# Performance work log

Measured on AMD Instinct MI355X. Metric: run time of the kernel, lower is better.

## Reference

```python
import jax, jax.numpy as jnp
import numpy as np

NEG_BIG = -1e9


def setup_inputs() -> dict:
    key = jax.random.key(0)
    ks = jax.random.split(key, 6)
    B, Tq, Tv, D, A = 4, 256, 1024, 512, 128
    inputs = jax.random.normal(ks[0], (B, Tv, D), dtype=jnp.float32)
    context = jax.random.normal(ks[1], (B, Tq, D), dtype=jnp.float32)
    mask = jnp.ones((B, Tv), dtype=jnp.int32)  # 1 = valid position
    scale = 1.0 / np.sqrt(D)
    Wk = jax.random.normal(ks[2], (D, A), dtype=jnp.float32) * scale
    bk = jnp.zeros((A,), dtype=jnp.float32)
    Wq = jax.random.normal(ks[3], (D, A), dtype=jnp.float32) * scale
    bq = jnp.zeros((A,), dtype=jnp.float32)
    attn_v = jax.random.normal(ks[4], (A,), dtype=jnp.float32) * (1.0 / np.sqrt(A))
    return {"inputs": inputs, "context": context, "mask": mask,
            "Wk": Wk, "bk": bk, "Wq": Wq, "bq": bq, "attn_v": attn_v}


def reference(inputs, context, mask, Wk, bk, Wq, bq, attn_v):
    # inputs: [B,Tv,D] (keys/values), context: [B,Tq,D] (queries)
    k = jnp.einsum('bvd,da->bva', inputs, Wk) + bk        # [B,Tv,A]
    q = jnp.einsum('bqd,da->bqa', context, Wq) + bq       # [B,Tq,A]
    # additive (Bahdanau) score: sum_a v_a * tanh(q + k)
    t = jnp.tanh(q[:, :, None, :] + k[:, None, :, :])     # [B,Tq,Tv,A]
    scores = jnp.einsum('bqva,a->bqv', t, attn_v)         # [B,Tq,Tv]
    neg = (1.0 - mask.astype(jnp.float32))[:, None, :] * NEG_BIG
    scores = scores + neg
    attn = jax.nn.softmax(scores, axis=-1)                # [B,Tq,Tv]
    return jnp.einsum('bqv,bvd->bqd', attn, inputs)       # [B,Tq,D]
```

## Files before the change

### kernel.cpp

```cpp
#include <hip/hip_runtime.h>
#include <math.h>

#define B   4
#define TQ  256
#define TV  1024
#define D   512
#define A   128

#define LOG2E     1.4426950408889634f
#define TWO_LOG2E 2.8853900817779268f
#define NEG_BIG_F (-1e9f)

#define QBLK (B * TQ / 8)
#define KBLK (B * TV / 8)

__global__ __launch_bounds__(256, 4) void proj_exp_kernel(
    const float* __restrict__ ctx, const float* __restrict__ inp,
    const float* __restrict__ Wq, const float* __restrict__ bq,
    const float* __restrict__ Wk, const float* __restrict__ bk,
    float* __restrict__ Eq, float* __restrict__ EkT) {
  __shared__ float ps[8][4][A];
  __shared__ float es[A][9];

  bool isQ = blockIdx.x < QBLK;
  const float* X; const float* W; const float* bias; int r0;
  if (isQ) { X = ctx; W = Wq; bias = bq; r0 = blockIdx.x * 8; }
  else     { X = inp; W = Wk; bias = bk; r0 = (blockIdx.x - QBLK) * 8; }

  int tid = threadIdx.x;
  int ap = (tid & 63) * 2;
  int g  = tid >> 6;

  int dbase = __builtin_amdgcn_readfirstlane(g * 128);
  const float* Xr = X + (size_t)r0 * D + dbase;
  const float* Wd = W + (size_t)dbase * A + ap;

  float2 acc[8];
#pragma unroll
  for (int j = 0; j < 8; ++j) acc[j] = make_float2(0.f, 0.f);

#pragma unroll 2
  for (int dd = 0; dd < 128; dd += 4) {
    float2 w0 = *(const float2*)(Wd + (size_t)(dd + 0) * A);
    float2 w1 = *(const float2*)(Wd + (size_t)(dd + 1) * A);
    float2 w2 = *(const float2*)(Wd + (size_t)(dd + 2) * A);
    float2 w3 = *(const float2*)(Wd + (size_t)(dd + 3) * A);
    float4 x[8];
#pragma unroll
    for (int j = 0; j < 8; ++j)
      x[j] = *(const float4*)(Xr + (size_t)j * D + dd);
#pragma unroll
    for (int j = 0; j < 8; ++j) {
      acc[j].x = fmaf(x[j].x, w0.x, acc[j].x);
      acc[j].y = fmaf(x[j].x, w0.y, acc[j].y);
      acc[j].x = fmaf(x[j].y, w1.x, acc[j].x);
      acc[j].y = fmaf(x[j].y, w1.y, acc[j].y);
      acc[j].x = fmaf(x[j].z, w2.x, acc[j].x);
      acc[j].y = fmaf(x[j].z, w2.y, acc[j].y);
      acc[j].x = fmaf(x[j].w, w3.x, acc[j].x);
      acc[j].y = fmaf(x[j].w, w3.y, acc[j].y);
    }
  }

#pragma unroll
  for (int j = 0; j < 8; ++j)
    *(float2*)&ps[j][g][ap] = acc[j];
  __syncthreads();

  int j  = tid >> 5;
  int a4 = (tid & 31) * 4;
  float4 p0 = *(const float4*)&ps[j][0][a4];
  float4 p1 = *(const float4*)&ps[j][1][a4];
  float4 p2 = *(const float4*)&ps[j][2][a4];
  float4 p3 = *(const float4*)&ps[j][3][a4];
  float4 bz = *(const float4*)(bias + a4);
  float4 ev;
  ev.x = __builtin_amdgcn_exp2f((((p0.x + p1.x) + (p2.x + p3.x)) + bz.x) * TWO_LOG2E);
  ev.y = __builtin_amdgcn_exp2f((((p0.y + p1.y) + (p2.y + p3.y)) + bz.y) * TWO_LOG2E);
  ev.z = __builtin_amdgcn_exp2f((((p0.z + p1.z) + (p2.z + p3.z)) + bz.z) * TWO_LOG2E);
  ev.w = __builtin_amdgcn_exp2f((((p0.w + p1.w) + (p2.w + p3.w)) + bz.w) * TWO_LOG2E);

  if (isQ) {
    *(float4*)(Eq + (size_t)(r0 + j) * A + a4) = ev;
  } else {
    es[a4 + 0][j] = ev.x;
    es[a4 + 1][j] = ev.y;
    es[a4 + 2][j] = ev.z;
    es[a4 + 3][j] = ev.w;
    __syncthreads();
    int b  = r0 >> 10;
    int v0 = r0 & (TV - 1);
    for (int i = tid; i < A * 8; i += 256) {
      int aa = i >> 3, jj = i & 7;
      EkT[((size_t)b * A + aa) * TV + v0 + jj] = es[aa][jj];
    }
  }
}

__global__ __launch_bounds__(512, 4) void score_softmax_kernel(
    const float* __restrict__ Eq, const float* __restrict__ EkT,
    const float* __restrict__ attn_v, const int* __restrict__ mask,
    float* __restrict__ attn) {
  __shared__ float redA[8], redB[8];
  __shared__ float bc[4];

  int tid = threadIdx.x;
  int v0  = (tid & 63) * 2 + (tid >> 6) * 128;
  int r0  = blockIdx.x * 2;
  int b   = r0 >> 8;

  const float* eqA = Eq + (size_t)r0 * A;
  const float* eqB = eqA + A;

  float sumV = 0.f;
#pragma unroll 16
  for (int i = 0; i < A; ++i) sumV += attn_v[i];

  const float* ekb = EkT + (size_t)b * A * TV + v0;
  float2 tA = make_float2(0.f, 0.f);
  float2 tB = make_float2(0.f, 0.f);

  float2 c0 = *(const float2*)(ekb + (size_t)0 * TV);
  float2 c1 = *(const float2*)(ekb + (size_t)1 * TV);
  float2 c2 = *(const float2*)(ekb + (size_t)2 * TV);
  float2 c3 = *(const float2*)(ekb + (size_t)3 * TV);

  for (int i = 0; i < A; i += 4) {
    float2 n0, n1, n2, n3;
    if (i < A - 4) {
      n0 = *(const float2*)(ekb + (size_t)(i + 4) * TV);
      n1 = *(const float2*)(ekb + (size_t)(i + 5) * TV);
      n2 = *(const float2*)(ekb + (size_t)(i + 6) * TV);
      n3 = *(const float2*)(ekb + (size_t)(i + 7) * TV);
    }
    float av0 = attn_v[i + 0], av1 = attn_v[i + 1];
    float av2 = attn_v[i + 2], av3 = attn_v[i + 3];
    float qa0 = eqA[i + 0], qa1 = eqA[i + 1], qa2 = eqA[i + 2], qa3 = eqA[i + 3];
    float qb0 = eqB[i + 0], qb1 = eqB[i + 1], qb2 = eqB[i + 2], qb3 = eqB[i + 3];

    tA.x = fmaf(av0, __builtin_amdgcn_rcpf(fmaf(c0.x, qa0, 1.f)), tA.x);
    tA.y = fmaf(av0, __builtin_amdgcn_rcpf(fmaf(c0.y, qa0, 1.f)), tA.y);
    tB.x = fmaf(av0, __builtin_amdgcn_rcpf(fmaf(c0.x, qb0, 1.f)), tB.x);
    tB.y = fmaf(av0, __builtin_amdgcn_rcpf(fmaf(c0.y, qb0, 1.f)), tB.y);

    tA.x = fmaf(av1, __builtin_amdgcn_rcpf(fmaf(c1.x, qa1, 1.f)), tA.x);
    tA.y = fmaf(av1, __builtin_amdgcn_rcpf(fmaf(c1.y, qa1, 1.f)), tA.y);
    tB.x = fmaf(av1, __builtin_amdgcn_rcpf(fmaf(c1.x, qb1, 1.f)), tB.x);
    tB.y = fmaf(av1, __builtin_amdgcn_rcpf(fmaf(c1.y, qb1, 1.f)), tB.y);

    tA.x = fmaf(av2, __builtin_amdgcn_rcpf(fmaf(c2.x, qa2, 1.f)), tA.x);
    tA.y = fmaf(av2, __builtin_amdgcn_rcpf(fmaf(c2.y, qa2, 1.f)), tA.y);
    tB.x = fmaf(av2, __builtin_amdgcn_rcpf(fmaf(c2.x, qb2, 1.f)), tB.x);
    tB.y = fmaf(av2, __builtin_amdgcn_rcpf(fmaf(c2.y, qb2, 1.f)), tB.y);

    tA.x = fmaf(av3, __builtin_amdgcn_rcpf(fmaf(c3.x, qa3, 1.f)), tA.x);
    tA.y = fmaf(av3, __builtin_amdgcn_rcpf(fmaf(c3.y, qa3, 1.f)), tA.y);
    tB.x = fmaf(av3, __builtin_amdgcn_rcpf(fmaf(c3.x, qb3, 1.f)), tB.x);
    tB.y = fmaf(av3, __builtin_amdgcn_rcpf(fmaf(c3.y, qb3, 1.f)), tB.y);

    c0 = n0; c1 = n1; c2 = n2; c3 = n3;
  }

  int2 mk = *(const int2*)(mask + b * TV + v0);
  float mkx = (1.f - (float)mk.x) * NEG_BIG_F;
  float mky = (1.f - (float)mk.y) * NEG_BIG_F;
  float2 sA, sB;
  sA.x = sumV - 2.f * tA.x + mkx;
  sA.y = sumV - 2.f * tA.y + mky;
  sB.x = sumV - 2.f * tB.x + mkx;
  sB.y = sumV - 2.f * tB.y + mky;

  float mA = fmaxf(sA.x, sA.y);
  float mB = fmaxf(sB.x, sB.y);
  for (int off = 32; off > 0; off >>= 1) {
    mA = fmaxf(mA, __shfl_down(mA, off, 64));
    mB = fmaxf(mB, __shfl_down(mB, off, 64));
  }
  int w = tid >> 6;
  if ((tid & 63) == 0) { redA[w] = mA; redB[w] = mB; }
  __syncthreads();
  if (tid == 0) {
    float a = redA[0], bm = redB[0];
#pragma unroll
    for (int i = 1; i < 8; ++i) { a = fmaxf(a, redA[i]); bm = fmaxf(bm, redB[i]); }
    bc[0] = a; bc[1] = bm;
  }
  __syncthreads();
  float MA = bc[0], MB = bc[1];

  float2 eAv, eBv;
  eAv.x = __builtin_amdgcn_exp2f((sA.x - MA) * LOG2E);
  eAv.y = __builtin_amdgcn_exp2f((sA.y - MA) * LOG2E);
  eBv.x = __builtin_amdgcn_exp2f((sB.x - MB) * LOG2E);
  eBv.y = __builtin_amdgcn_exp2f((sB.y - MB) * LOG2E);
  float lA = eAv.x + eAv.y;
  float lB = eBv.x + eBv.y;
  for (int off = 32; off > 0; off >>= 1) {
    lA += __shfl_down(lA, off, 64);
    lB += __shfl_down(lB, off, 64);
  }
  __syncthreads();
  if ((tid & 63) == 0) { redA[w] = lA; redB[w] = lB; }
  __syncthreads();
  if (tid == 0) {
    float a = 0.f, bs = 0.f;
#pragma unroll
    for (int i = 0; i < 8; ++i) { a += redA[i]; bs += redB[i]; }
    bc[2] = a; bc[3] = bs;
  }
  __syncthreads();
  float iA = 1.f / bc[2];
  float iB = 1.f / bc[3];

  *(float2*)(attn + (size_t)r0 * TV + v0) =
      make_float2(eAv.x * iA, eAv.y * iA);
  *(float2*)(attn + (size_t)(r0 + 1) * TV + v0) =
      make_float2(eBv.x * iB, eBv.y * iB);
}

__global__ __launch_bounds__(512, 4) void pv_kernel(
    const float* __restrict__ attn, const float* __restrict__ X,
    float* __restrict__ out) {
  __shared__ float lds[8 * 1024];
  int dt = blockIdx.x;
  int q0 = blockIdx.y * 8;
  int b  = q0 >> 8;
  int tid  = threadIdx.x;
  int w    = tid >> 6;
  int lane = tid & 63;
  int col  = lane & 31;
  int qh   = lane >> 5;
  int d0 = dt * 128 + col * 4;

  {
    const float4* src = (const float4*)(attn + (size_t)q0 * TV);
    float4* dst = (float4*)lds;
    for (int i = tid; i < 8 * 256; i += 512) dst[i] = src[i];
  }
  __syncthreads();

  float4 acc[4];
#pragma unroll
  for (int j = 0; j < 4; ++j) acc[j] = make_float4(0.f, 0.f, 0.f, 0.f);

  int vbase = w * 128;
  const float* Xb = X + ((size_t)b * TV + vbase) * D + d0;
  const float* arow = &lds[(qh * 4) * 1024 + vbase];

  float4 xc0 = *(const float4*)(Xb + (size_t)0 * D);
  float4 xc1 = *(const float4*)(Xb + (size_t)1 * D);
  float4 xc2 = *(const float4*)(Xb + (size_t)2 * D);
  float4 xc3 = *(const float4*)(Xb + (size_t)3 * D);

  for (int vi = 0; vi < 128; vi += 4) {
    float4 xn0, xn1, xn2, xn3;
    if (vi < 124) {
      const float* Xn = Xb + (size_t)(vi + 4) * D;
      xn0 = *(const float4*)(Xn + (size_t)0 * D);
      xn1 = *(const float4*)(Xn + (size_t)1 * D);
      xn2 = *(const float4*)(Xn + (size_t)2 * D);
      xn3 = *(const float4*)(Xn + (size_t)3 * D);
    }
#pragma unroll
    for (int j = 0; j < 4; ++j) {
      float4 av = *(const float4*)(arow + j * 1024 + vi);
      acc[j].x = fmaf(av.x, xc0.x, acc[j].x);
      acc[j].y = fmaf(av.x, xc0.y, acc[j].y);
      acc[j].z = fmaf(av.x, xc0.z, acc[j].z);
      acc[j].w = fmaf(av.x, xc0.w, acc[j].w);
      acc[j].x = fmaf(av.y, xc1.x, acc[j].x);
      acc[j].y = fmaf(av.y, xc1.y, acc[j].y);
      acc[j].z = fmaf(av.y, xc1.z, acc[j].z);
      acc[j].w = fmaf(av.y, xc1.w, acc[j].w);
      acc[j].x = fmaf(av.z, xc2.x, acc[j].x);
      acc[j].y = fmaf(av.z, xc2.y, acc[j].y);
      acc[j].z = fmaf(av.z, xc2.z, acc[j].z);
      acc[j].w = fmaf(av.z, xc2.w, acc[j].w);
      acc[j].x = fmaf(av.w, xc3.x, acc[j].x);
      acc[j].y = fmaf(av.w, xc3.y, acc[j].y);
      acc[j].z = fmaf(av.w, xc3.z, acc[j].z);
      acc[j].w = fmaf(av.w, xc3.w, acc[j].w);
    }
    xc0 = xn0; xc1 = xn1; xc2 = xn2; xc3 = xn3;
  }

  __syncthreads();

  {
    float4* pat = (float4*)lds + (size_t)w * 256;
#pragma unroll
    for (int j = 0; j < 4; ++j)
      pat[(qh * 4 + j) * 32 + col] = acc[j];
  }
  __syncthreads();

  if (tid < 256) {
    int row = tid >> 5;
    int c   = tid & 31;
    const float4* p = (const float4*)lds + tid;
    float4 r = p[0];
#pragma unroll
    for (int i = 1; i < 8; ++i) {
      float4 t = p[(size_t)i * 256];
      r.x += t.x; r.y += t.y; r.z += t.z; r.w += t.w;
    }
    *(float4*)(out + (size_t)(q0 + row) * D + dt * 128 + c * 4) = r;
  }
}

extern "C" void kernel_launch(void* const* d_in, const int* in_sizes, int n_in,
                              void* d_out, int out_size, void* d_ws, size_t ws_size,
                              hipStream_t stream) {
  const float* inputs  = (const float*)d_in[0];
  const float* context = (const float*)d_in[1];
  const int*   mask    = (const int*)d_in[2];
  const float* Wk      = (const float*)d_in[3];
  const float* bk      = (const float*)d_in[4];
  const float* Wq      = (const float*)d_in[5];
  const float* bq      = (const float*)d_in[6];
  const float* attn_v  = (const float*)d_in[7];
  float* out = (float*)d_out;

  float* Eq   = (float*)d_ws;
  float* EkT  = Eq + B * TQ * A;
  float* attn = EkT + (size_t)B * A * TV;

  proj_exp_kernel<<<QBLK + KBLK, 256, 0, stream>>>(context, inputs, Wq, bq,
                                                   Wk, bk, Eq, EkT);
  score_softmax_kernel<<<B * TQ / 2, 512, 0, stream>>>(Eq, EkT, attn_v, mask,
                                                       attn);
  pv_kernel<<<dim3(4, 128), 512, 0, stream>>>(attn, inputs, out);
}
```

Before: 135.2 us.

## Restructure PV kernel: wave-uniform attn reads, wider d tiles, fewer blocks

The PV kernel no longer stages the 8x1024 attention tile in LDS. Each wave now reads its four attention rows straight from global memory, using wave-uniform addresses so the loads are effectively scalar, and prefetches them along with X. Each block covers 256 output columns instead of 128, so the grid is halved and X is re-read from global half as often across blocks. The split-K reduction now combines 4 partials instead of 8, which shrinks the LDS footprint. The trade-offs are fewer blocks (256) for the GPU to occupy its CUs and longer per-wave loops of 256 v steps.

```diff
diff --git a/kernel.cpp b/kernel.cpp
--- a/kernel.cpp
+++ b/kernel.cpp
@@ -221,90 +221,88 @@
 __global__ __launch_bounds__(512, 4) void pv_kernel(
     const float* __restrict__ attn, const float* __restrict__ X,
     float* __restrict__ out) {
-  __shared__ float lds[8 * 1024];
+  __shared__ float4 ps[4][8][64];
   int dt = blockIdx.x;
   int q0 = blockIdx.y * 8;
   int b  = q0 >> 8;
   int tid  = threadIdx.x;
   int w    = tid >> 6;
   int lane = tid & 63;
-  int col  = lane & 31;
-  int qh   = lane >> 5;
-  int d0 = dt * 128 + col * 4;
-
-  {
-    const float4* src = (const float4*)(attn + (size_t)q0 * TV);
-    float4* dst = (float4*)lds;
-    for (int i = tid; i < 8 * 256; i += 512) dst[i] = src[i];
-  }
-  __syncthreads();
+  int qr  = __builtin_amdgcn_readfirstlane((w & 1) * 4);
+  int vch = __builtin_amdgcn_readfirstlane(w >> 1);
+  int d0 = dt * 256 + lane * 4;
+
+  const float* Xb   = X + ((size_t)b * TV + vch * 256) * D + d0;
+  const float* arow = attn + (size_t)(q0 + qr) * TV + vch * 256;
 
   float4 acc[4];
 #pragma unroll
   for (int j = 0; j < 4; ++j) acc[j] = make_float4(0.f, 0.f, 0.f, 0.f);
-
-  int vbase = w * 128;
-  const float* Xb = X + ((size_t)b * TV + vbase) * D + d0;
-  const float* arow = &lds[(qh * 4) * 1024 + vbase];
 
   float4 xc0 = *(const float4*)(Xb + (size_t)0 * D);
   float4 xc1 = *(const float4*)(Xb + (size_t)1 * D);
   float4 xc2 = *(const float4*)(Xb + (size_t)2 * D);
   float4 xc3 = *(const float4*)(Xb + (size_t)3 * D);
-
-  for (int vi = 0; vi < 128; vi += 4) {
-    float4 xn0, xn1, xn2, xn3;
-    if (vi < 124) {
+  float4 ac0 = *(const float4*)(arow + (size_t)0 * TV);
+  float4 ac1 = *(const float4*)(arow + (size_t)1 * TV);
+  float4 ac2 = *(const float4*)(arow + (size_t)2 * TV);
+  float4 ac3 = *(const float4*)(arow + (size_t)3 * TV);
+
+  for (int vi = 0; vi < 256; vi += 4) {
+    float4 xn0, xn1, xn2, xn3, an0, an1, an2, an3;
+    if (vi < 252) {
       const float* Xn = Xb + (size_t)(vi + 4) * D;
       xn0 = *(const float4*)(Xn + (size_t)0 * D);
       xn1 = *(const float4*)(Xn + (size_t)1 * D);
       xn2 = *(const float4*)(Xn + (size_t)2 * D);
       xn3 = *(const float4*)(Xn + (size_t)3 * D);
+      an0 = *(const float4*)(arow + (size_t)0 * TV + vi + 4);
+      an1 = *(const float4*)(arow + (size_t)1 * TV + vi + 4);
+      an2 = *(const float4*)(arow + (size_t)2 * TV + vi + 4);
+      an3 = *(const float4*)(arow + (size_t)3 * TV + vi + 4);
     }
 #pragma unroll
     for (int j = 0; j < 4; ++j) {
-      float4 av = *(const float4*)(arow + j * 1024 + vi);
-      acc[j].x = fmaf(av.x, xc0.x, acc[j].x);
-      acc[j].y = fmaf(av.x, xc0.y, acc[j].y);
-      acc[j].z = fmaf(av.x, xc0.z, acc[j].z);
-      acc[j].w = fmaf(av.x, xc0.w, acc[j].w);
-      acc[j].x = fmaf(av.y, xc1.x, acc[j].x);
-      acc[j].y = fmaf(av.y, xc1.y, acc[j].y);
-      acc[j].z = fmaf(av.y, xc1.z, acc[j].z);
-      acc[j].w = fmaf(av.y, xc1.w, acc[j].w);
-      acc[j].x = fmaf(av.z, xc2.x, acc[j].x);
-      acc[j].y = fmaf(av.z, xc2.y, acc[j].y);
-      acc[j].z = fmaf(av.z, xc2.z, acc[j].z);
-      acc[j].w = fmaf(av.z, xc2.w, acc[j].w);
-      acc[j].x = fmaf(av.w, xc3.x, acc[j].x);
-      acc[j].y = fmaf(av.w, xc3.y, acc[j].y);
-      acc[j].z = fmaf(av.w, xc3.z, acc[j].z);
-      acc[j].w = fmaf(av.w, xc3.w, acc[j].w);
+      float4 a = (j == 0) ? ac0 : (j == 1) ? ac1 : (j == 2) ? ac2 : ac3;
+      acc[j].x = fmaf(a.x, xc0.x, acc[j].x);
+      acc[j].y = fmaf(a.x, xc0.y, acc[j].y);
+      acc[j].z = fmaf(a.x, xc0.z, acc[j].z);
+      acc[j].w = fmaf(a.x, xc0.w, acc[j].w);
+      acc[j].x = fmaf(a.y, xc1.x, acc[j].x);
+      acc[j].y = fmaf(a.y, xc1.y, acc[j].y);
+      acc[j].z = fmaf(a.y, xc1.z, acc[j].z);
+      acc[j].w = fmaf(a.y, xc1.w, acc[j].w);
+      acc[j].x = fmaf(a.z, xc2.x, acc[j].x);
+      acc[j].y = fmaf(a.z, xc2.y, acc[j].y);
+      acc[j].z = fmaf(a.z, xc2.z, acc[j].z);
+      acc[j].w = fmaf(a.z, xc2.w, acc[j].w);
+      acc[j].x = fmaf(a.w, xc3.x, acc[j].x);
+      acc[j].y = fmaf(a.w, xc3.y, acc[j].y);
+      acc[j].z = fmaf(a.w, xc3.z, acc[j].z);
+      acc[j].w = fmaf(a.w, xc3.w, acc[j].w);
     }
     xc0 = xn0; xc1 = xn1; xc2 = xn2; xc3 = xn3;
-  }
-
+    ac0 = an0; ac1 = an1; ac2 = an2; ac3 = an3;
+  }
+
+#pragma unroll
+  for (int j = 0; j < 4; ++j)
+    ps[vch][qr + j][lane] = acc[j];
   __syncthreads();
 
   {
-    float4* pat = (float4*)lds + (size_t)w * 256;
-#pragma unroll
-    for (int j = 0; j < 4; ++j)
-      pat[(qh * 4 + j) * 32 + col] = acc[j];
-  }
-  __syncthreads();
-
-  if (tid < 256) {
-    int row = tid >> 5;
-    int c   = tid & 31;
-    const float4* p = (const float4*)lds + tid;
-    float4 r = p[0];
-#pragma unroll
-    for (int i = 1; i < 8; ++i) {
-      float4 t = p[(size_t)i * 256];
-      r.x += t.x; r.y += t.y; r.z += t.z; r.w += t.w;
-    }
-    *(float4*)(out + (size_t)(q0 + row) * D + dt * 128 + c * 4) = r;
+    int row = tid >> 6;
+    int c   = tid & 63;
+    float4 r0v = ps[0][row][c];
+    float4 r1v = ps[1][row][c];
+    float4 r2v = ps[2][row][c];
+    float4 r3v = ps[3][row][c];
+    float4 r;
+    r.x = (r0v.x + r1v.x) + (r2v.x + r3v.x);
+    r.y = (r0v.y + r1v.y) + (r2v.y + r3v.y);
+    r.z = (r0v.z + r1v.z) + (r2v.z + r3v.z);
+    r.w = (r0v.w + r1v.w) + (r2v.w + r3v.w);
+    *(float4*)(out + (size_t)(q0 + row) * D + dt * 256 + c * 4) = r;
   }
 }
 
@@ -329,5 +327,5 @@
                                                    Wk, bk, Eq, EkT);
   score_softmax_kernel<<<B * TQ / 2, 512, 0, stream>>>(Eq, EkT, attn_v, mask,
                                                        attn);
-  pv_kernel<<<dim3(4, 128), 512, 0, stream>>>(attn, inputs, out);
+  pv_kernel<<<dim3(2, 128), 512, 0, stream>>>(attn, inputs, out);
 }
```

New measurement: 137.3 us. About the same (+1.5%).
